# Optimization experiments

Measured on AMD Instinct MI355X. Metric: run time of the kernel, lower is better.

Reference implementation:

```python
import jax, jax.numpy as jnp
import numpy as np

N_EMBD = 2048
N_HEAD = 16
HEAD_DIM = 128


def setup_inputs() -> dict:
    key = jax.random.key(0)
    ks = jax.random.split(key, 9)
    B, S = 2, 2048
    s_in = 1.0 / np.sqrt(N_EMBD)
    s_out = 1.0 / np.sqrt(N_HEAD * HEAD_DIM)
    return {
        "x": jax.random.normal(ks[0], (B, S, N_EMBD), dtype=jnp.float32),
        "Wq": jax.random.uniform(ks[1], (N_HEAD * HEAD_DIM, N_EMBD), jnp.float32, -s_in, s_in),
        "bq": jax.random.uniform(ks[2], (N_HEAD * HEAD_DIM,), jnp.float32, -s_in, s_in),
        "Wk": jax.random.uniform(ks[3], (HEAD_DIM, N_EMBD), jnp.float32, -s_in, s_in),
        "bk": jax.random.uniform(ks[4], (HEAD_DIM,), jnp.float32, -s_in, s_in),
        "Wv": jax.random.uniform(ks[5], (HEAD_DIM, N_EMBD), jnp.float32, -s_in, s_in),
        "bv": jax.random.uniform(ks[6], (HEAD_DIM,), jnp.float32, -s_in, s_in),
        "Wo": jax.random.uniform(ks[7], (N_EMBD, N_HEAD * HEAD_DIM), jnp.float32, -s_out, s_out),
        "bo": jax.random.uniform(ks[8], (N_EMBD,), jnp.float32, -s_out, s_out),
    }


def reference(x, Wq, bq, Wk, bk, Wv, bv, Wo, bo):
    B, S, E = x.shape
    H, D = N_HEAD, HEAD_DIM
    q = (x @ Wq.T + bq).reshape(B, S, H, D)        # [B,S,H,D]
    k = x @ Wk.T + bk                              # [B,S,D] shared across heads
    v = x @ Wv.T + bv                              # [B,S,D]
    scale = 1.0 / jnp.sqrt(jnp.asarray(D, x.dtype))
    # QK^T with shared K (no per-head expansion materialized)
    attn = jnp.einsum('bqhd,bkd->bhqk', q * scale, k)  # [B,H,S,S]
    # causal mask: positions j>i set to -inf (masked_fill where mask==0)
    causal = jnp.tril(jnp.ones((S, S), dtype=bool))
    attn = jnp.where(causal[None, None], attn, -jnp.inf)
    attn = jax.nn.softmax(attn, axis=-1)
    out = jnp.einsum('bhqk,bkd->bqhd', attn, v).reshape(B, S, H * D)
    return out @ Wo.T + bo
```

## Files before the change

### kernel.cpp

```cpp
#include <hip/hip_runtime.h>
#include <stdint.h>

typedef __attribute__((ext_vector_type(8))) short bf16x8;
typedef __attribute__((ext_vector_type(4))) float f32x4;
typedef __attribute__((ext_vector_type(4))) unsigned short u16x4;
typedef unsigned short u16;

__device__ __forceinline__ u16 f2bf(float f) {
  union { float f; unsigned u; } x; x.f = f;
  unsigned r = x.u + 0x7fffu + ((x.u >> 16) & 1u);
  return (u16)(r >> 16);
}

__device__ __forceinline__ void load16_lds(const void* g, void* l) {
  __builtin_amdgcn_global_load_lds((const __attribute__((address_space(1))) void*)g,
                                   (__attribute__((address_space(3))) void*)l, 16, 0, 0);
}

__global__ void cvt_all(const float* __restrict__ x, const float* __restrict__ wq,
                        const float* __restrict__ wk, const float* __restrict__ wv,
                        const float* __restrict__ wo,
                        u16* __restrict__ xb, u16* __restrict__ wqb,
                        u16* __restrict__ wkb, u16* __restrict__ wvb,
                        u16* __restrict__ wob) {
  int i = blockIdx.x * 256 + threadIdx.x;
  const float* src; u16* dst; int off;
  if (i < 2097152)      { src = x;  dst = xb;  off = 0; }
  else if (i < 3145728) { src = wq; dst = wqb; off = 2097152; }
  else if (i < 3211264) { src = wk; dst = wkb; off = 3145728; }
  else if (i < 3276800) { src = wv; dst = wvb; off = 3211264; }
  else                  { src = wo; dst = wob; off = 3276800; }
  int j = i - off;
  f32x4 f = ((const f32x4*)src)[j];
  u16x4 o;
  o.x = f2bf(f.x); o.y = f2bf(f.y); o.z = f2bf(f.z); o.w = f2bf(f.w);
  ((u16x4*)dst)[j] = o;
}

__global__ void gemm_qkv(const u16* __restrict__ X, const u16* __restrict__ Wq,
                         const u16* __restrict__ Wk, const u16* __restrict__ Wv,
                         const float* __restrict__ bq, const float* __restrict__ bk,
                         const float* __restrict__ bv, u16* __restrict__ Y,
                         u16* __restrict__ Vt) {
  constexpr int K = 2048, LDY = 2176;
  __shared__ __align__(16) u16 At[128 * 64];
  __shared__ __align__(16) u16 Bt[128 * 64];
  const int bm = blockIdx.x & 31;
  const int bn = blockIdx.x >> 5;
  const int m0 = bm * 128;
  const u16* Wsrc; int nbase;
  if (bn < 16)      { Wsrc = Wq; nbase = bn * 128; }
  else if (bn == 16){ Wsrc = Wk; nbase = 0; }
  else              { Wsrc = Wv; nbase = 0; }
  const int tid = threadIdx.x, wid = tid >> 6, lane = tid & 63;
  const int quad = lane >> 4, l16 = lane & 15;
  const int wm = wid >> 1, wn = wid & 1;
  f32x4 acc[4][4] = {};
  for (int k0 = 0; k0 < K; k0 += 64) {
    __syncthreads();
#pragma unroll
    for (int t = 0; t < 4; t++) {
      int c = t * 256 + tid;
      int row = c >> 3, skc = c & 7, kc = skc ^ (row & 7);
      load16_lds(X + (size_t)(m0 + row) * K + k0 + kc * 8, At + (size_t)(t * 256 + wid * 64) * 8);
      load16_lds(Wsrc + (size_t)(nbase + row) * K + k0 + kc * 8, Bt + (size_t)(t * 256 + wid * 64) * 8);
    }
    asm volatile("s_waitcnt vmcnt(0)" ::: "memory");
    __syncthreads();
#pragma unroll
    for (int ks = 0; ks < 2; ks++) {
      bf16x8 af[4], bfv[4];
#pragma unroll
      for (int mi = 0; mi < 4; mi++) {
        int row = wm * 64 + mi * 16 + l16;
        af[mi] = *(const bf16x8*)(At + (row * 8 + ((ks * 4 + quad) ^ (l16 & 7))) * 8);
      }
#pragma unroll
      for (int ni = 0; ni < 4; ni++) {
        int row = wn * 64 + ni * 16 + l16;
        bfv[ni] = *(const bf16x8*)(Bt + (row * 8 + ((ks * 4 + quad) ^ (l16 & 7))) * 8);
      }
#pragma unroll
      for (int mi = 0; mi < 4; mi++)
#pragma unroll
        for (int ni = 0; ni < 4; ni++)
          acc[mi][ni] = __builtin_amdgcn_mfma_f32_16x16x32_bf16(af[mi], bfv[ni], acc[mi][ni], 0, 0, 0);
    }
  }
  if (bn == 17) {
    int bb = m0 >> 11;
#pragma unroll
    for (int ni = 0; ni < 4; ni++) {
      int d = wn * 64 + ni * 16 + l16;
      float bias = bv[d];
#pragma unroll
      for (int mi = 0; mi < 4; mi++) {
        int m = m0 + wm * 64 + mi * 16 + quad * 4;
        u16x4 pk;
        pk.x = f2bf(acc[mi][ni][0] + bias);
        pk.y = f2bf(acc[mi][ni][1] + bias);
        pk.z = f2bf(acc[mi][ni][2] + bias);
        pk.w = f2bf(acc[mi][ni][3] + bias);
        *(u16x4*)(Vt + (size_t)(bb * 128 + d) * 2048 + (m & 2047)) = pk;
      }
    }
  } else {
    const float* bs = (bn < 16) ? bq : bk;
    const int cbase = (bn < 16) ? bn * 128 : 2048;
    const int bbase = (bn < 16) ? bn * 128 : 0;
#pragma unroll
    for (int ni = 0; ni < 4; ni++) {
      int nl = wn * 64 + ni * 16 + l16;
      float bias = bs[bbase + nl];
#pragma unroll
      for (int mi = 0; mi < 4; mi++) {
        int m = m0 + wm * 64 + mi * 16 + quad * 4;
#pragma unroll
        for (int r = 0; r < 4; r++)
          Y[(size_t)(m + r) * LDY + cbase + nl] = f2bf(acc[mi][ni][r] + bias);
      }
    }
  }
}

__global__ __launch_bounds__(128, 2) void flash_mqa(const u16* __restrict__ Y,
                                                    const u16* __restrict__ Vt,
                                                    u16* __restrict__ O) {
  constexpr int LDY = 2176, S = 2048, D = 128;
  __shared__ __align__(16) u16 Kt[64 * 128];
  __shared__ __align__(16) u16 Vts[128 * 64];
  __shared__ __align__(16) u16 Pl[2][32 * 64];
  const int bid = blockIdx.x;
  const int u = bid & 255, k4 = bid >> 8;
  const int w8 = u >> 5, bh = u & 31;
  int qt;
  switch (k4) { case 0: qt = w8; break;  case 1: qt = 31 - w8; break;
                case 2: qt = w8 + 8; break; default: qt = 23 - w8; }
  const int b = bh >> 4, h = bh & 15;
  const int q0 = qt * 64;
  const int tid = threadIdx.x, wid = tid >> 6, lane = tid & 63;
  const int quad = lane >> 4, l16 = lane & 15;
  const float c1 = 0.08838834764831845f * 1.4426950408889634f;
  const float c2 = 8.0f * 1.4426950408889634f;
  bf16x8 qf[2][4];
#pragma unroll
  for (int a = 0; a < 2; a++) {
    const u16* qrow = Y + (size_t)(b * S + q0 + wid * 32 + a * 16 + l16) * LDY + h * D;
#pragma unroll
    for (int kd = 0; kd < 4; kd++) qf[a][kd] = *(const bf16x8*)(qrow + kd * 32 + quad * 8);
  }
  f32x4 oacc[2][8] = {};
  float ls[2][4] = {};
  const int nkt = qt + 1;
  for (int kt = 0; kt < nkt; kt++) {
    const int k0 = kt * 64;
    const bool last = (kt == nkt - 1);
    __syncthreads();
#pragma unroll
    for (int t = 0; t < 8; t++) {
      int c = t * 128 + tid;
      int j = c >> 4, dc = (c & 15) ^ (j & 15);
      load16_lds(Y + (size_t)(b * S + k0 + j) * LDY + 2048 + dc * 8,
                 Kt + (size_t)(t * 128 + wid * 64) * 8);
    }
#pragma unroll
    for (int t = 0; t < 8; t++) {
      int c = t * 128 + tid;
      int d = c >> 3, jc = (c & 7) ^ (d & 7);
      load16_lds(Vt + (size_t)(b * D + d) * S + k0 + jc * 8,
                 Vts + (size_t)(t * 128 + wid * 64) * 8);
    }
    asm volatile("s_waitcnt vmcnt(0)" ::: "memory");
    __syncthreads();
    f32x4 sc[2][4] = {};
#pragma unroll
    for (int kd = 0; kd < 4; kd++) {
      int dch = kd * 4 + quad;
#pragma unroll
      for (int jf = 0; jf < 4; jf++) {
        bf16x8 bb = *(const bf16x8*)(Kt + ((size_t)(jf * 16 + l16) * 16 + (dch ^ l16)) * 8);
        sc[0][jf] = __builtin_amdgcn_mfma_f32_16x16x32_bf16(qf[0][kd], bb, sc[0][jf], 0, 0, 0);
        sc[1][jf] = __builtin_amdgcn_mfma_f32_16x16x32_bf16(qf[1][kd], bb, sc[1][jf], 0, 0, 0);
      }
    }
#pragma unroll
    for (int a = 0; a < 2; a++) {
#pragma unroll
      for (int r = 0; r < 4; r++) {
        float v[4];
#pragma unroll
        for (int jf = 0; jf < 4; jf++) v[jf] = sc[a][jf][r];
        if (last) {
          int i = q0 + wid * 32 + a * 16 + quad * 4 + r;
#pragma unroll
          for (int jf = 0; jf < 4; jf++)
            if (k0 + jf * 16 + l16 > i) v[jf] = -1e30f;
        }
        float p[4];
#pragma unroll
        for (int jf = 0; jf < 4; jf++) p[jf] = __builtin_amdgcn_exp2f(v[jf] * c1 - c2);
        ls[a][r] += (p[0] + p[1]) + (p[2] + p[3]);
        int m = a * 16 + quad * 4 + r;
#pragma unroll
        for (int jf = 0; jf < 4; jf++) {
          int jc = jf * 2 + (l16 >> 3);
          Pl[wid][((size_t)m * 8 + (jc ^ (m & 7))) * 8 + (l16 & 7)] = f2bf(p[jf]);
        }
      }
    }
    asm volatile("s_waitcnt lgkmcnt(0)" ::: "memory");
#pragma unroll
    for (int cch = 0; cch < 2; cch++) {
      int jcr = cch * 4 + quad;
      bf16x8 pa0 = *(const bf16x8*)(&Pl[wid][((size_t)l16 * 8 + (jcr ^ (l16 & 7))) * 8]);
      bf16x8 pa1 = *(const bf16x8*)(&Pl[wid][((size_t)(16 + l16) * 8 + (jcr ^ (l16 & 7))) * 8]);
#pragma unroll
      for (int nd = 0; nd < 8; nd++) {
        int d = nd * 16 + l16;
        bf16x8 vb = *(const bf16x8*)(Vts + ((size_t)d * 8 + (jcr ^ (d & 7))) * 8);
        oacc[0][nd] = __builtin_amdgcn_mfma_f32_16x16x32_bf16(pa0, vb, oacc[0][nd], 0, 0, 0);
        oacc[1][nd] = __builtin_amdgcn_mfma_f32_16x16x32_bf16(pa1, vb, oacc[1][nd], 0, 0, 0);
      }
    }
  }
#pragma unroll
  for (int a = 0; a < 2; a++) {
#pragma unroll
    for (int r = 0; r < 4; r++) {
      float s = ls[a][r];
#pragma unroll
      for (int off = 1; off < 16; off <<= 1) s += __shfl_xor(s, off, 64);
      float inv = 1.f / s;
      int tok = q0 + wid * 32 + a * 16 + quad * 4 + r;
      u16* orow = O + (size_t)(b * S + tok) * 2048 + h * D;
#pragma unroll
      for (int nd = 0; nd < 8; nd++)
        orow[nd * 16 + l16] = f2bf(oacc[a][nd][r] * inv);
    }
  }
}

__global__ void gemm_out(const u16* __restrict__ A, const u16* __restrict__ W,
                         const float* __restrict__ bias, float* __restrict__ Cout) {
  constexpr int K = 2048, N = 2048;
  __shared__ __align__(16) u16 At[128 * 64];
  __shared__ __align__(16) u16 Bt[128 * 64];
  const int bm = blockIdx.x & 31;
  const int bn = blockIdx.x >> 5;
  const int m0 = bm * 128, n0 = bn * 128;
  const int tid = threadIdx.x, wid = tid >> 6, lane = tid & 63;
  const int quad = lane >> 4, l16 = lane & 15;
  const int wm = wid >> 1, wn = wid & 1;
  f32x4 acc[4][4] = {};
  for (int k0 = 0; k0 < K; k0 += 64) {
    __syncthreads();
#pragma unroll
    for (int t = 0; t < 4; t++) {
      int c = t * 256 + tid;
      int row = c >> 3, kc = (c & 7) ^ (row & 7);
      load16_lds(A + (size_t)(m0 + row) * K + k0 + kc * 8, At + (size_t)(t * 256 + wid * 64) * 8);
      load16_lds(W + (size_t)(n0 + row) * K + k0 + kc * 8, Bt + (size_t)(t * 256 + wid * 64) * 8);
    }
    asm volatile("s_waitcnt vmcnt(0)" ::: "memory");
    __syncthreads();
#pragma unroll
    for (int ks = 0; ks < 2; ks++) {
      bf16x8 af[4], bfv[4];
#pragma unroll
      for (int mi = 0; mi < 4; mi++) {
        int row = wm * 64 + mi * 16 + l16;
        af[mi] = *(const bf16x8*)(At + (row * 8 + ((ks * 4 + quad) ^ (l16 & 7))) * 8);
      }
#pragma unroll
      for (int ni = 0; ni < 4; ni++) {
        int row = wn * 64 + ni * 16 + l16;
        bfv[ni] = *(const bf16x8*)(Bt + (row * 8 + ((ks * 4 + quad) ^ (l16 & 7))) * 8);
      }
#pragma unroll
      for (int mi = 0; mi < 4; mi++)
#pragma unroll
        for (int ni = 0; ni < 4; ni++)
          acc[mi][ni] = __builtin_amdgcn_mfma_f32_16x16x32_bf16(af[mi], bfv[ni], acc[mi][ni], 0, 0, 0);
    }
  }
#pragma unroll
  for (int ni = 0; ni < 4; ni++) {
    int n = n0 + wn * 64 + ni * 16 + l16;
    float bv = bias[n];
#pragma unroll
    for (int mi = 0; mi < 4; mi++) {
      int m = m0 + wm * 64 + mi * 16 + quad * 4;
#pragma unroll
      for (int r = 0; r < 4; r++)
        Cout[(size_t)(m + r) * N + n] = acc[mi][ni][r] + bv;
    }
  }
}

extern "C" void kernel_launch(void* const* d_in, const int* in_sizes, int n_in,
                              void* d_out, int out_size, void* d_ws, size_t ws_size,
                              hipStream_t stream) {
  (void)in_sizes; (void)n_in; (void)out_size; (void)ws_size;
  const float* x  = (const float*)d_in[0];
  const float* Wq = (const float*)d_in[1];
  const float* bq = (const float*)d_in[2];
  const float* Wk = (const float*)d_in[3];
  const float* bk = (const float*)d_in[4];
  const float* Wv = (const float*)d_in[5];
  const float* bv = (const float*)d_in[6];
  const float* Wo = (const float*)d_in[7];
  const float* bo = (const float*)d_in[8];
  float* out = (float*)d_out;

  char* ws = (char*)d_ws;
  size_t off = 0;
  auto carve = [&](size_t bytes) -> char* {
    char* p = ws + off; off += (bytes + 255) & ~(size_t)255; return p;
  };
  u16* xb  = (u16*)carve((size_t)4096 * 2048 * 2);
  u16* wqb = (u16*)carve((size_t)2048 * 2048 * 2);
  u16* wkb = (u16*)carve((size_t)128 * 2048 * 2);
  u16* wvb = (u16*)carve((size_t)128 * 2048 * 2);
  u16* wob = (u16*)carve((size_t)2048 * 2048 * 2);
  u16* Yb  = (u16*)carve((size_t)4096 * 2176 * 2);
  u16* Vtb = (u16*)carve((size_t)2 * 128 * 2048 * 2);
  u16* Ob  = (u16*)carve((size_t)4096 * 2048 * 2);

  cvt_all<<<16896, 256, 0, stream>>>(x, Wq, Wk, Wv, Wo, xb, wqb, wkb, wvb, wob);
  gemm_qkv<<<576, 256, 0, stream>>>(xb, wqb, wkb, wvb, bq, bk, bv, Yb, Vtb);
  flash_mqa<<<1024, 128, 0, stream>>>(Yb, Vtb, Ob);
  gemm_out<<<512, 256, 0, stream>>>(Ob, wob, bo, out);
}
```

Measured before the change: 280.8 us.

## Split flash attention KV range across two blocks and add combine kernel

Each query tile's key range is split into two halves handled by separate blocks, which write unnormalized bf16 partial outputs and row sums to workspace. A new combine kernel sums the partials and normalizes them. Blocks are now ordered longest-first. The goal is to double the parallelism and shorten the critical path of the longest causal tiles. The cost is extra partial-output traffic, an additional kernel launch, and bf16 rounding of unnormalized partials. Combining without a running max is still valid because the kernel uses a fixed exponent offset rather than an online max.

```diff
diff --git a/kernel.cpp b/kernel.cpp
--- a/kernel.cpp
+++ b/kernel.cpp
@@ -125,19 +125,19 @@
 
 __global__ __launch_bounds__(128, 2) void flash_mqa(const u16* __restrict__ Y,
                                                     const u16* __restrict__ Vt,
-                                                    u16* __restrict__ O) {
+                                                    u16* __restrict__ Op,
+                                                    float* __restrict__ lp) {
   constexpr int LDY = 2176, S = 2048, D = 128;
   __shared__ __align__(16) u16 Kt[64 * 128];
   __shared__ __align__(16) u16 Vts[128 * 64];
   __shared__ __align__(16) u16 Pl[2][32 * 64];
   const int bid = blockIdx.x;
-  const int u = bid & 255, k4 = bid >> 8;
-  const int w8 = u >> 5, bh = u & 31;
-  int qt;
-  switch (k4) { case 0: qt = w8; break;  case 1: qt = 31 - w8; break;
-                case 2: qt = w8 + 8; break; default: qt = 23 - w8; }
+  const int qt = 31 - (bid >> 6);
+  const int rem = bid & 63, bh = rem >> 1, half = rem & 1;
   const int b = bh >> 4, h = bh & 15;
   const int q0 = qt * 64;
+  const int ntiles = qt + 1, h1 = (ntiles + 1) >> 1;
+  const int kt0 = half ? h1 : 0, kt1 = half ? ntiles : h1;
   const int tid = threadIdx.x, wid = tid >> 6, lane = tid & 63;
   const int quad = lane >> 4, l16 = lane & 15;
   const float c1 = 0.08838834764831845f * 1.4426950408889634f;
@@ -151,10 +151,9 @@
   }
   f32x4 oacc[2][8] = {};
   float ls[2][4] = {};
-  const int nkt = qt + 1;
-  for (int kt = 0; kt < nkt; kt++) {
+  for (int kt = kt0; kt < kt1; kt++) {
     const int k0 = kt * 64;
-    const bool last = (kt == nkt - 1);
+    const bool diag = (kt == qt);
     __syncthreads();
 #pragma unroll
     for (int t = 0; t < 8; t++) {
@@ -190,7 +189,7 @@
         float v[4];
 #pragma unroll
         for (int jf = 0; jf < 4; jf++) v[jf] = sc[a][jf][r];
-        if (last) {
+        if (diag) {
           int i = q0 + wid * 32 + a * 16 + quad * 4 + r;
 #pragma unroll
           for (int jf = 0; jf < 4; jf++)
@@ -223,6 +222,8 @@
       }
     }
   }
+  u16* Oph = Op + (size_t)half * 8388608;
+  float* lph = lp + (size_t)half * 65536;
 #pragma unroll
   for (int a = 0; a < 2; a++) {
 #pragma unroll
@@ -230,14 +231,38 @@
       float s = ls[a][r];
 #pragma unroll
       for (int off = 1; off < 16; off <<= 1) s += __shfl_xor(s, off, 64);
-      float inv = 1.f / s;
       int tok = q0 + wid * 32 + a * 16 + quad * 4 + r;
-      u16* orow = O + (size_t)(b * S + tok) * 2048 + h * D;
+      u16* orow = Oph + (size_t)(b * S + tok) * 2048 + h * D;
 #pragma unroll
       for (int nd = 0; nd < 8; nd++)
-        orow[nd * 16 + l16] = f2bf(oacc[a][nd][r] * inv);
-    }
-  }
+        orow[nd * 16 + l16] = f2bf(oacc[a][nd][r]);
+      if (l16 == 0) lph[(size_t)(b * S + tok) * 16 + h] = s;
+    }
+  }
+}
+
+__global__ void combine(const u16* __restrict__ Op, const float* __restrict__ lp,
+                        u16* __restrict__ Ob) {
+  int i = blockIdx.x * 256 + threadIdx.x;
+  size_t e = (size_t)i * 8;
+  int row = i >> 8;
+  int h = (i & 255) >> 4;
+  float la = lp[(size_t)row * 16 + h], lb = lp[65536 + (size_t)row * 16 + h];
+  float inv = 1.0f / (la + lb);
+  uint4 pa = *(const uint4*)(Op + e);
+  uint4 pb = *(const uint4*)(Op + 8388608 + e);
+  const unsigned* ua = (const unsigned*)&pa;
+  const unsigned* ub = (const unsigned*)&pb;
+  u16 outv[8];
+#pragma unroll
+  for (int k = 0; k < 4; k++) {
+    union { unsigned u; float f; } a0, a1, b0, b1;
+    a0.u = (ua[k] & 0xffffu) << 16;  a1.u = ua[k] & 0xffff0000u;
+    b0.u = (ub[k] & 0xffffu) << 16;  b1.u = ub[k] & 0xffff0000u;
+    outv[k * 2]     = f2bf((a0.f + b0.f) * inv);
+    outv[k * 2 + 1] = f2bf((a1.f + b1.f) * inv);
+  }
+  *(uint4*)(Ob + e) = *(uint4*)outv;
 }
 
 __global__ void gemm_out(const u16* __restrict__ A, const u16* __restrict__ W,
@@ -325,9 +350,12 @@
   u16* Yb  = (u16*)carve((size_t)4096 * 2176 * 2);
   u16* Vtb = (u16*)carve((size_t)2 * 128 * 2048 * 2);
   u16* Ob  = (u16*)carve((size_t)4096 * 2048 * 2);
+  u16* Opart = (u16*)carve((size_t)2 * 4096 * 2048 * 2);
+  float* lpart = (float*)carve((size_t)2 * 4096 * 16 * 4);
 
   cvt_all<<<16896, 256, 0, stream>>>(x, Wq, Wk, Wv, Wo, xb, wqb, wkb, wvb, wob);
   gemm_qkv<<<576, 256, 0, stream>>>(xb, wqb, wkb, wvb, bq, bk, bv, Yb, Vtb);
-  flash_mqa<<<1024, 128, 0, stream>>>(Yb, Vtb, Ob);
+  flash_mqa<<<2048, 128, 0, stream>>>(Yb, Vtb, Opart, lpart);
+  combine<<<4096, 256, 0, stream>>>(Opart, lpart, Ob);
   gemm_out<<<512, 256, 0, stream>>>(Ob, wob, bo, out);
 }
```

Result: faster. 268.0 us (-4.5%).
